# Kernel tuning notes

Hardware: AMD Instinct MI355X
Metric: run time of the kernel (lower is better)

## Reference

```python
import jax, jax.numpy as jnp
import numpy as np

EMBED_DIM = 1024
NUM_HEADS = 16
HEAD_DIM = EMBED_DIM // NUM_HEADS

# Hamilton-product combination tensor C[out_comp, weight_comp, in_comp]
_C = np.zeros((4, 4, 4), dtype=np.float32)
for o, terms in enumerate([
    [(0, 0, 1), (1, 1, -1), (2, 2, -1), (3, 3, -1)],  # r_out
    [(1, 0, 1), (0, 1, 1), (3, 2, 1), (2, 3, -1)],    # i_out
    [(2, 0, 1), (3, 1, -1), (0, 2, 1), (1, 3, 1)],    # j_out
    [(3, 0, 1), (2, 1, 1), (1, 2, -1), (0, 3, 1)],    # k_out
]):
    for d, c, s in terms:
        _C[o, d, c] = s
C = jnp.asarray(_C)


def _xavier(key, shape):
    fan_in, fan_out = shape[-1], shape[-2]
    a = jnp.sqrt(6.0 / (fan_in + fan_out))
    return jax.random.uniform(key, shape, jnp.float32, -a, a)


def setup_inputs() -> dict:
    key = jax.random.key(0)
    ks = jax.random.split(key, 8)
    B, T, E = 4, 1024, EMBED_DIM
    inp = {
        'q': jax.random.normal(ks[0], (B, T, E, 4), jnp.float32),
        'k': jax.random.normal(ks[1], (B, T, E, 4), jnp.float32),
        'v': jax.random.normal(ks[2], (B, T, E, 4), jnp.float32),
    }
    for name, kk in zip(['Wq', 'Wk', 'Wv', 'Wo'], ks[3:7]):
        # stacked [r,i,j,k] weights, each (out_features, in_features)
        inp[name] = _xavier(kk, (4, E, E))
        inp[name.replace('W', 'b')] = jnp.zeros((E, 4), jnp.float32)
    return inp


def qlinear(x, W, b):
    # x: [B,T,in,4(c)], W: [4(d),out,in], b: [out,4]
    # effective block weight: Weff[q_out, c_in, out, in]
    Weff = jnp.einsum('doi,qdc->qcoi', W, C)
    out = jnp.einsum('btic,qcoi->btoq', x, Weff)
    return out + b  # bias broadcasts over B,T


def split_heads(x):
    B, T, D, Q = x.shape
    x = x.reshape(B, T, NUM_HEADS, HEAD_DIM, Q)
    return x.transpose(0, 2, 1, 3, 4)  # [B,H,T,hd,4]


def combine_heads(x):
    B, H, T, D, Q = x.shape
    return x.transpose(0, 2, 1, 3, 4).reshape(B, T, H * D, Q)


def reference(q, k, v, Wq, bq, Wk, bk, Wv, bv, Wo, bo):
    qh = split_heads(qlinear(q, Wq, bq))
    kh = split_heads(qlinear(k, Wk, bk))
    vh = split_heads(qlinear(v, Wv, bv))
    scale = 1.0 / jnp.sqrt(jnp.float32(HEAD_DIM * 4))
    scores = jnp.einsum('bhqfd,bhkfd->bhqk', qh, kh) * scale
    attn = jax.nn.softmax(scores, axis=-1)
    out = jnp.einsum('bhqk,bhkfd->bhqfd', attn, vh)
    return qlinear(combine_heads(out), Wo, bo)
```

## Files before the change

kernel.cpp:

```cpp
#include <hip/hip_runtime.h>
#include <hip/hip_bf16.h>

typedef _Float16 h16;
typedef h16   h16x8 __attribute__((ext_vector_type(8)));
typedef h16   h16x4 __attribute__((ext_vector_type(4)));
typedef float f32x4 __attribute__((ext_vector_type(4)));

#define EMB 1024
#define ED4 4096L

__device__ __forceinline__ void gload_lds16(const void* g, void* l) {
    __builtin_amdgcn_global_load_lds(
        (__attribute__((address_space(1))) void*)g,
        (__attribute__((address_space(3))) void*)l,
        16, 0, 0);
}

__global__ __launch_bounds__(256) void k_build_m(const float* __restrict__ W, h16* __restrict__ M) {
    int t = blockIdx.x * 256 + threadIdx.x;
    int i = t & 1023;
    int n = t >> 10;
    int o = n >> 2, q = n & 3;
    unsigned packed = 0xEu | (0x8u << 4) | (0x2u << 8) | (0x4u << 12);
    unsigned sm = (packed >> (q * 4)) & 0xFu;
    h16x4 out;
#pragma unroll
    for (int c = 0; c < 4; ++c) {
        int d = q ^ c;
        float w = W[((long)d * EMB + o) * EMB + i];
        out[c] = (h16)(((sm >> c) & 1u) ? -w : w);
    }
    *(h16x4*)&M[(long)n * ED4 + i * 4] = out;
}

__global__ __launch_bounds__(256) void k_f32_to_f16(const float* __restrict__ in, h16* __restrict__ out) {
    long i = ((long)blockIdx.x * 256 + threadIdx.x) * 4;
    float4 v = *(const float4*)(in + i);
    h16x4 o;
    o[0] = (h16)v.x; o[1] = (h16)v.y; o[2] = (h16)v.z; o[3] = (h16)v.w;
    *(h16x4*)(out + i) = o;
}

#define BAR() __builtin_amdgcn_s_barrier()
#define STAGE(matv, basev, row0v, tt, hh) do { \
    const h16* _src = (basev) + ((row0v) + (hh) * 128L) * 4096L + (long)(tt) * 64 + scol; \
    h16* _dst = &lds[(((tt) & 1) << 15) + (matv) * 16384 + (hh) * 8192 + w * 512]; \
    gload_lds16(_src, _dst); \
    gload_lds16(_src + 64 * 4096L, _dst + 4096); \
} while (0)
#define LDA_(mh, m, ks) (*(const h16x8*)&lds[cb + (mh) * 8192 + (wm * 64 + (m) * 16 + fr) * 64 + ((((ks) * 4 + kq) ^ fr7) << 3)])
#define LDB_(nh, n, ks) (*(const h16x8*)&lds[cb + 16384 + (nh) * 8192 + (wn * 32 + (n) * 16 + fr) * 64 + ((((ks) * 4 + kq) ^ fr7) << 3)])
#define MFMA_Q(MH, NH, BF) do { \
    __builtin_amdgcn_s_setprio(1); \
    _Pragma("unroll") \
    for (int m = 0; m < 4; ++m) \
        _Pragma("unroll") \
        for (int n = 0; n < 2; ++n) { \
            acc[MH][NH][m][n] = __builtin_amdgcn_mfma_f32_16x16x32_f16(af[m][0], BF[n][0], acc[MH][NH][m][n], 0, 0, 0); \
            acc[MH][NH][m][n] = __builtin_amdgcn_mfma_f32_16x16x32_f16(af[m][1], BF[n][1], acc[MH][NH][m][n], 0, 0, 0); \
        } \
    __builtin_amdgcn_s_setprio(0); \
} while (0)

template <typename OUT_T, bool VT>
__global__ __launch_bounds__(512, 2) void k_gemm256(
    const h16* __restrict__ A, const h16* __restrict__ B,
    OUT_T* __restrict__ C, const float* __restrict__ bias, int nt)
{
    __shared__ __align__(16) h16 lds[65536];

    const int tid = threadIdx.x;
    const int w  = tid >> 6, l = tid & 63;
    const int wm = w >> 2, wn = w & 3;
    const int fr = l & 15, fr7 = l & 7, kq = l >> 4;

    const int srow = w * 8 + (l >> 3);
    const int scol = ((l & 7) ^ ((l >> 3) & 7)) << 3;
    const long arow0 = (long)blockIdx.x * 256 + srow;
    const long brow0 = (long)blockIdx.y * 256 + srow;

    f32x4 acc[2][2][4][2] = {};

    STAGE(0, A, arow0, 0, 0);
    STAGE(1, B, brow0, 0, 0);
    STAGE(0, A, arow0, 0, 1);
    STAGE(1, B, brow0, 0, 1);
    STAGE(0, A, arow0, 1, 0);
    STAGE(1, B, brow0, 1, 0);
    asm volatile("s_waitcnt vmcnt(4)" ::: "memory");
    __builtin_amdgcn_sched_barrier(0);
    BAR();

    for (int t = 0; t < nt; ++t) {
        const int cb = (t & 1) << 15;
        h16x8 af[4][2], b0[2][2], b1[2][2];

#pragma unroll
        for (int m = 0; m < 4; ++m) { af[m][0] = LDA_(0, m, 0); af[m][1] = LDA_(0, m, 1); }
#pragma unroll
        for (int n = 0; n < 2; ++n) { b0[n][0] = LDB_(0, n, 0); b0[n][1] = LDB_(0, n, 1); }
#pragma unroll
        for (int n = 0; n < 2; ++n) { b1[n][0] = LDB_(1, n, 0); b1[n][1] = LDB_(1, n, 1); }
        if (t + 1 < nt) {
            STAGE(0, A, arow0, t + 1, 1);
            STAGE(1, B, brow0, t + 1, 1);
        }
        MFMA_Q(0, 0, b0);
        MFMA_Q(0, 1, b1);
        BAR();

#pragma unroll
        for (int m = 0; m < 4; ++m) { af[m][0] = LDA_(1, m, 0); af[m][1] = LDA_(1, m, 1); }
        if (t + 2 < nt) {
            STAGE(0, A, arow0, t + 2, 0);
            STAGE(1, B, brow0, t + 2, 0);
        }
        if (t < nt - 2) { asm volatile("s_waitcnt vmcnt(4)" ::: "memory"); }
        else            { asm volatile("s_waitcnt vmcnt(0)" ::: "memory"); }
        __builtin_amdgcn_sched_barrier(0);
        MFMA_Q(1, 0, b0);
        MFMA_Q(1, 1, b1);
        BAR();
    }

    const long row00 = (long)blockIdx.x * 256 + wm * 64 + kq * 4;
    const int  col00 = (int)blockIdx.y * 256 + wn * 32 + fr;
#pragma unroll
    for (int mh = 0; mh < 2; ++mh)
#pragma unroll
        for (int nh = 0; nh < 2; ++nh)
#pragma unroll
            for (int n = 0; n < 2; ++n) {
                const int col = col00 + nh * 128 + n * 16;
                const float bv = bias[col];
#pragma unroll
                for (int m = 0; m < 4; ++m) {
                    const long r0 = row00 + mh * 128 + m * 16;
                    if constexpr (VT) {
                        h16x4 o;
#pragma unroll
                        for (int j = 0; j < 4; ++j) o[j] = (h16)(acc[mh][nh][m][n][j] + bv);
                        const long zidx = (r0 >> 10) * 16 + (col >> 8);
                        *(h16x4*)((h16*)C + zidx * 262144L + (long)(col & 255) * 1024 + (r0 & 1023)) = o;
                    } else {
#pragma unroll
                        for (int j = 0; j < 4; ++j)
                            C[(r0 + j) * 4096L + col] = (OUT_T)(acc[mh][nh][m][n][j] + bv);
                    }
                }
            }
}

template <typename OUT_T, bool HAS_BIAS>
__global__ __launch_bounds__(256) void k_gemm_bt(
    const h16* __restrict__ A, const h16* __restrict__ B,
    OUT_T* __restrict__ C, const float* __restrict__ bias,
    int lda, int ldb, int ldc,
    long sAb, long sAh, long sBb, long sBh, long sCb, long sCh,
    float alpha, int kIters)
{
    __shared__ __align__(16) h16 As[128 * 32];
    __shared__ __align__(16) h16 Bs[128 * 32];

    const int z = blockIdx.z, zb = z >> 4, zh = z & 15;
    const h16* Ab = A + zb * sAb + zh * sAh + (long)blockIdx.x * 128 * lda;
    const h16* Bb = B + zb * sBb + zh * sBh + (long)blockIdx.y * 128 * ldb;

    const int tid = threadIdx.x, w = tid >> 6, lane = tid & 63;
    const int wr = (w >> 1) * 64, wc = (w & 1) * 64;
    const int scol = (((lane & 3) ^ ((lane >> 3) & 3)) * 8);
    const int srow = lane >> 2;
    const int fr   = lane & 15;
    const int koff = (((lane >> 4) ^ ((fr >> 1) & 3)) * 8);

    f32x4 acc[4][4] = {};

    for (int kt = 0; kt < kIters; ++kt) {
        const int k0 = kt * 32;
#pragma unroll
        for (int j = 0; j < 2; ++j) {
            const int ca  = w * 2 + j;
            const int row = ca * 16 + srow;
            gload_lds16(Ab + (long)row * lda + k0 + scol, &As[ca * 512]);
            gload_lds16(Bb + (long)row * ldb + k0 + scol, &Bs[ca * 512]);
        }
        __syncthreads();

        h16x8 af[4], bfr[4];
#pragma unroll
        for (int m = 0; m < 4; ++m)
            af[m] = *(const h16x8*)&As[(wr + m * 16 + fr) * 32 + koff];
#pragma unroll
        for (int n = 0; n < 4; ++n)
            bfr[n] = *(const h16x8*)&Bs[(wc + n * 16 + fr) * 32 + koff];
        __syncthreads();

#pragma unroll
        for (int m = 0; m < 4; ++m)
#pragma unroll
            for (int n = 0; n < 4; ++n)
                acc[m][n] = __builtin_amdgcn_mfma_f32_16x16x32_f16(af[m], bfr[n], acc[m][n], 0, 0, 0);
    }

    OUT_T* Cb = C + zb * sCb + zh * sCh;
    const long rbase = (long)blockIdx.x * 128 + wr + (lane >> 4) * 4;
    const int  cbase = blockIdx.y * 128 + wc + fr;
#pragma unroll
    for (int n = 0; n < 4; ++n) {
        const int col = cbase + n * 16;
        const float bv = HAS_BIAS ? bias[col] : 0.0f;
#pragma unroll
        for (int m = 0; m < 4; ++m) {
            const long row0 = rbase + m * 16;
#pragma unroll
            for (int j = 0; j < 4; ++j) {
                float vv = acc[m][n][j] * alpha + bv;
                Cb[(row0 + j) * ldc + col] = (OUT_T)vv;
            }
        }
    }
}

__global__ __launch_bounds__(256) void k_softmax(h16* __restrict__ S) {
    const long row = blockIdx.x;
    h16* p = S + row * 1024;
    const int tid = threadIdx.x, w = tid >> 6, lane = tid & 63;
    h16x4 xi = *(const h16x4*)&p[tid * 4];
    float x[4];
#pragma unroll
    for (int j = 0; j < 4; ++j) x[j] = (float)xi[j];
    float m = fmaxf(fmaxf(x[0], x[1]), fmaxf(x[2], x[3]));
#pragma unroll
    for (int off = 32; off; off >>= 1) m = fmaxf(m, __shfl_xor(m, off));
    __shared__ float red[8];
    if (lane == 0) red[w] = m;
    __syncthreads();
    m = fmaxf(fmaxf(red[0], red[1]), fmaxf(red[2], red[3]));
    float s = 0.0f;
#pragma unroll
    for (int j = 0; j < 4; ++j) { x[j] = __expf(x[j] - m); s += x[j]; }
#pragma unroll
    for (int off = 32; off; off >>= 1) s += __shfl_xor(s, off);
    if (lane == 0) red[4 + w] = s;
    __syncthreads();
    s = red[4] + red[5] + red[6] + red[7];
    const float inv = 1.0f / s;
    h16x4 o;
#pragma unroll
    for (int j = 0; j < 4; ++j) o[j] = (h16)(x[j] * inv);
    *(h16x4*)&p[tid * 4] = o;
}

extern "C" void kernel_launch(void* const* d_in, const int* in_sizes, int n_in,
                              void* d_out, int out_size, void* d_ws, size_t ws_size,
                              hipStream_t stream) {
    const float* q  = (const float*)d_in[0];
    const float* k  = (const float*)d_in[1];
    const float* v  = (const float*)d_in[2];
    const float* Wq = (const float*)d_in[3];
    const float* bq = (const float*)d_in[4];
    const float* Wk = (const float*)d_in[5];
    const float* bk = (const float*)d_in[6];
    const float* Wv = (const float*)d_in[7];
    const float* bv = (const float*)d_in[8];
    const float* Wo = (const float*)d_in[9];
    const float* bo = (const float*)d_in[10];
    float* out = (float*)d_out;

    char* ws = (char*)d_ws;
    const long MB = 1024L * 1024;
    h16* X  = (h16*)(ws + 0 * MB);
    h16* M  = (h16*)(ws + 32 * MB);
    h16* Qb = (h16*)(ws + 64 * MB);
    h16* Kb = (h16*)(ws + 96 * MB);
    h16* Vt = (h16*)(ws + 128 * MB);
    h16* AO = (h16*)(ws + 160 * MB);
    h16* Sc = (h16*)(ws + 192 * MB);

    dim3 blk(256);
    dim3 g256(16, 16, 1);

    k_f32_to_f16<<<16384, blk, 0, stream>>>(q, X);
    k_build_m<<<16384, blk, 0, stream>>>(Wq, M);
    k_gemm256<h16, false><<<g256, 512, 0, stream>>>(X, M, Qb, bq, 64);

    k_f32_to_f16<<<16384, blk, 0, stream>>>(k, X);
    k_build_m<<<16384, blk, 0, stream>>>(Wk, M);
    k_gemm256<h16, false><<<g256, 512, 0, stream>>>(X, M, Kb, bk, 64);

    k_f32_to_f16<<<16384, blk, 0, stream>>>(v, X);
    k_build_m<<<16384, blk, 0, stream>>>(Wv, M);
    k_gemm256<h16, true><<<g256, 512, 0, stream>>>(X, M, Vt, bv, 64);

    for (int c = 0; c < 4; ++c) {
        const h16* Qc  = Qb + (long)c * 1024 * 4096;
        const h16* Kc  = Kb + (long)c * 1024 * 4096;
        const h16* VtC = Vt + (long)c * 16 * 256 * 1024;
        h16*       AOc = AO + (long)c * 1024 * 4096;

        k_gemm_bt<h16, false><<<dim3(8, 8, 16), blk, 0, stream>>>(
            Qc, Kc, Sc, nullptr,
            4096, 4096, 1024,
            0, 256,
            0, 256,
            0, 1024L * 1024,
            0.0625f, 8);

        k_softmax<<<16384, blk, 0, stream>>>(Sc);

        k_gemm_bt<h16, false><<<dim3(8, 2, 16), blk, 0, stream>>>(
            Sc, VtC, AOc, nullptr,
            1024, 1024, 4096,
            0, 1024L * 1024,
            0, 256L * 1024,
            0, 256,
            1.0f, 32);
    }

    k_build_m<<<16384, blk, 0, stream>>>(Wo, M);
    k_gemm256<float, false><<<g256, 512, 0, stream>>>(AO, M, out, bo, 64);
}
```

Before: 865.7 us.

## Generalize 256-tile GEMM to batched strides and use it for attention scores

The 256x256 MFMA GEMM kernel gains lda/ldb/ldc, per-batch and per-head strides, an alpha scale and an optional bias. This lets it compute the Q·K^T score matrices in place of the smaller 128-tile kernel. The attention loop now processes two batch elements per iteration (32 heads per launch) instead of one, which halves the number of score, softmax and P·V launches. In exchange, the score buffer doubles in size, and with K=256 the big-tile kernel runs only four iterations, so its pipeline prologue is a larger share of its work.

```diff
diff --git a/kernel.cpp b/kernel.cpp
--- a/kernel.cpp
+++ b/kernel.cpp
@@ -42,11 +42,11 @@
 }
 
 #define BAR() __builtin_amdgcn_s_barrier()
-#define STAGE(matv, basev, row0v, tt, hh) do { \
-    const h16* _src = (basev) + ((row0v) + (hh) * 128L) * 4096L + (long)(tt) * 64 + scol; \
+#define STAGE(matv, basev, row0v, ldv, tt, hh) do { \
+    const h16* _src = (basev) + ((row0v) + (hh) * 128L) * (ldv) + (long)(tt) * 64 + scol; \
     h16* _dst = &lds[(((tt) & 1) << 15) + (matv) * 16384 + (hh) * 8192 + w * 512]; \
     gload_lds16(_src, _dst); \
-    gload_lds16(_src + 64 * 4096L, _dst + 4096); \
+    gload_lds16(_src + 64 * (long)(ldv), _dst + 4096); \
 } while (0)
 #define LDA_(mh, m, ks) (*(const h16x8*)&lds[cb + (mh) * 8192 + (wm * 64 + (m) * 16 + fr) * 64 + ((((ks) * 4 + kq) ^ fr7) << 3)])
 #define LDB_(nh, n, ks) (*(const h16x8*)&lds[cb + 16384 + (nh) * 8192 + (wn * 32 + (n) * 16 + fr) * 64 + ((((ks) * 4 + kq) ^ fr7) << 3)])
@@ -62,10 +62,13 @@
     __builtin_amdgcn_s_setprio(0); \
 } while (0)
 
-template <typename OUT_T, bool VT>
+template <typename OUT_T, bool VT, bool HAS_BIAS>
 __global__ __launch_bounds__(512, 2) void k_gemm256(
     const h16* __restrict__ A, const h16* __restrict__ B,
-    OUT_T* __restrict__ C, const float* __restrict__ bias, int nt)
+    OUT_T* __restrict__ C, const float* __restrict__ bias,
+    int lda, int ldb, int ldc,
+    long sAb, long sAh, long sBb, long sBh, long sCb, long sCh,
+    float alpha, int nt)
 {
     __shared__ __align__(16) h16 lds[65536];
 
@@ -74,6 +77,10 @@
     const int wm = w >> 2, wn = w & 3;
     const int fr = l & 15, fr7 = l & 7, kq = l >> 4;
 
+    const int z = blockIdx.z, zb = z >> 4, zh = z & 15;
+    const h16* Ab = A + zb * sAb + zh * sAh;
+    const h16* Bb = B + zb * sBb + zh * sBh;
+
     const int srow = w * 8 + (l >> 3);
     const int scol = ((l & 7) ^ ((l >> 3) & 7)) << 3;
     const long arow0 = (long)blockIdx.x * 256 + srow;
@@ -81,12 +88,12 @@
 
     f32x4 acc[2][2][4][2] = {};
 
-    STAGE(0, A, arow0, 0, 0);
-    STAGE(1, B, brow0, 0, 0);
-    STAGE(0, A, arow0, 0, 1);
-    STAGE(1, B, brow0, 0, 1);
-    STAGE(0, A, arow0, 1, 0);
-    STAGE(1, B, brow0, 1, 0);
+    STAGE(0, Ab, arow0, lda, 0, 0);
+    STAGE(1, Bb, brow0, ldb, 0, 0);
+    STAGE(0, Ab, arow0, lda, 0, 1);
+    STAGE(1, Bb, brow0, ldb, 0, 1);
+    STAGE(0, Ab, arow0, lda, 1, 0);
+    STAGE(1, Bb, brow0, ldb, 1, 0);
     asm volatile("s_waitcnt vmcnt(4)" ::: "memory");
     __builtin_amdgcn_sched_barrier(0);
     BAR();
@@ -102,8 +109,8 @@
 #pragma unroll
         for (int n = 0; n < 2; ++n) { b1[n][0] = LDB_(1, n, 0); b1[n][1] = LDB_(1, n, 1); }
         if (t + 1 < nt) {
-            STAGE(0, A, arow0, t + 1, 1);
-            STAGE(1, B, brow0, t + 1, 1);
+            STAGE(0, Ab, arow0, lda, t + 1, 1);
+            STAGE(1, Bb, brow0, ldb, t + 1, 1);
         }
         MFMA_Q(0, 0, b0);
         MFMA_Q(0, 1, b1);
@@ -112,8 +119,8 @@
 #pragma unroll
         for (int m = 0; m < 4; ++m) { af[m][0] = LDA_(1, m, 0); af[m][1] = LDA_(1, m, 1); }
         if (t + 2 < nt) {
-            STAGE(0, A, arow0, t + 2, 0);
-            STAGE(1, B, brow0, t + 2, 0);
+            STAGE(0, Ab, arow0, lda, t + 2, 0);
+            STAGE(1, Bb, brow0, ldb, t + 2, 0);
         }
         if (t < nt - 2) { asm volatile("s_waitcnt vmcnt(4)" ::: "memory"); }
         else            { asm volatile("s_waitcnt vmcnt(0)" ::: "memory"); }
@@ -123,6 +130,7 @@
         BAR();
     }
 
+    OUT_T* Cb = C + zb * sCb + zh * sCh;
     const long row00 = (long)blockIdx.x * 256 + wm * 64 + kq * 4;
     const int  col00 = (int)blockIdx.y * 256 + wn * 32 + fr;
 #pragma unroll
@@ -132,20 +140,20 @@
 #pragma unroll
             for (int n = 0; n < 2; ++n) {
                 const int col = col00 + nh * 128 + n * 16;
-                const float bv = bias[col];
+                const float bv = HAS_BIAS ? bias[col] : 0.0f;
 #pragma unroll
                 for (int m = 0; m < 4; ++m) {
                     const long r0 = row00 + mh * 128 + m * 16;
                     if constexpr (VT) {
                         h16x4 o;
 #pragma unroll
-                        for (int j = 0; j < 4; ++j) o[j] = (h16)(acc[mh][nh][m][n][j] + bv);
+                        for (int j = 0; j < 4; ++j) o[j] = (h16)(acc[mh][nh][m][n][j] * alpha + bv);
                         const long zidx = (r0 >> 10) * 16 + (col >> 8);
-                        *(h16x4*)((h16*)C + zidx * 262144L + (long)(col & 255) * 1024 + (r0 & 1023)) = o;
+                        *(h16x4*)((h16*)Cb + zidx * 262144L + (long)(col & 255) * 1024 + (r0 & 1023)) = o;
                     } else {
 #pragma unroll
                         for (int j = 0; j < 4; ++j)
-                            C[(r0 + j) * 4096L + col] = (OUT_T)(acc[mh][nh][m][n][j] + bv);
+                            Cb[(r0 + j) * (long)ldc + col] = (OUT_T)(acc[mh][nh][m][n][j] * alpha + bv);
                     }
                 }
             }
@@ -282,41 +290,45 @@
 
     k_f32_to_f16<<<16384, blk, 0, stream>>>(q, X);
     k_build_m<<<16384, blk, 0, stream>>>(Wq, M);
-    k_gemm256<h16, false><<<g256, 512, 0, stream>>>(X, M, Qb, bq, 64);
+    k_gemm256<h16, false, true><<<g256, 512, 0, stream>>>(
+        X, M, Qb, bq, 4096, 4096, 4096, 0, 0, 0, 0, 0, 0, 1.0f, 64);
 
     k_f32_to_f16<<<16384, blk, 0, stream>>>(k, X);
     k_build_m<<<16384, blk, 0, stream>>>(Wk, M);
-    k_gemm256<h16, false><<<g256, 512, 0, stream>>>(X, M, Kb, bk, 64);
+    k_gemm256<h16, false, true><<<g256, 512, 0, stream>>>(
+        X, M, Kb, bk, 4096, 4096, 4096, 0, 0, 0, 0, 0, 0, 1.0f, 64);
 
     k_f32_to_f16<<<16384, blk, 0, stream>>>(v, X);
     k_build_m<<<16384, blk, 0, stream>>>(Wv, M);
-    k_gemm256<h16, true><<<g256, 512, 0, stream>>>(X, M, Vt, bv, 64);
-
-    for (int c = 0; c < 4; ++c) {
-        const h16* Qc  = Qb + (long)c * 1024 * 4096;
-        const h16* Kc  = Kb + (long)c * 1024 * 4096;
-        const h16* VtC = Vt + (long)c * 16 * 256 * 1024;
-        h16*       AOc = AO + (long)c * 1024 * 4096;
-
-        k_gemm_bt<h16, false><<<dim3(8, 8, 16), blk, 0, stream>>>(
+    k_gemm256<h16, true, true><<<g256, 512, 0, stream>>>(
+        X, M, Vt, bv, 4096, 4096, 4096, 0, 0, 0, 0, 0, 0, 1.0f, 64);
+
+    for (int c = 0; c < 2; ++c) {
+        const h16* Qc  = Qb + (long)c * 2 * 1024 * 4096;
+        const h16* Kc  = Kb + (long)c * 2 * 1024 * 4096;
+        const h16* VtC = Vt + (long)c * 32 * 262144;
+        h16*       AOc = AO + (long)c * 2 * 1024 * 4096;
+
+        k_gemm256<h16, false, false><<<dim3(4, 4, 32), 512, 0, stream>>>(
             Qc, Kc, Sc, nullptr,
             4096, 4096, 1024,
-            0, 256,
-            0, 256,
-            0, 1024L * 1024,
-            0.0625f, 8);
-
-        k_softmax<<<16384, blk, 0, stream>>>(Sc);
-
-        k_gemm_bt<h16, false><<<dim3(8, 2, 16), blk, 0, stream>>>(
+            1024L * 4096, 256,
+            1024L * 4096, 256,
+            16L * 1024 * 1024, 1024L * 1024,
+            0.0625f, 4);
+
+        k_softmax<<<32768, blk, 0, stream>>>(Sc);
+
+        k_gemm_bt<h16, false><<<dim3(8, 2, 32), blk, 0, stream>>>(
             Sc, VtC, AOc, nullptr,
             1024, 1024, 4096,
-            0, 1024L * 1024,
-            0, 256L * 1024,
-            0, 256,
+            16L * 1024 * 1024, 1024L * 1024,
+            16L * 262144, 262144,
+            1024L * 4096, 256,
             1.0f, 32);
     }
 
     k_build_m<<<16384, blk, 0, stream>>>(Wo, M);
-    k_gemm256<float, false><<<g256, 512, 0, stream>>>(AO, M, out, bo, 64);
-}
+    k_gemm256<float, false, true><<<g256, 512, 0, stream>>>(
+        AO, M, out, bo, 4096, 4096, 4096, 0, 0, 0, 0, 0, 0, 1.0f, 64);
+}
```

Measured after the change: 813.7 us. -6.0%, faster.
